# Optimization experiments

Measured on AMD Instinct MI355X. Metric: run time of the kernel, lower is better.

Reference implementation:

```python
import jax, jax.numpy as jnp
import numpy as np

D_MODEL = 256
N_HEADS = 4
WINDOW = 8
DECAY = 0.9
STEP_SIZE = 0.5


def _linear(x, w, b):
    # torch nn.Linear: y = x @ w.T + b, w: [out, in]
    return jnp.einsum('...i,oi->...o', x, w) + b


def _layernorm(x, scale, bias, eps=1e-5):
    mu = jnp.mean(x, axis=-1, keepdims=True)
    var = jnp.var(x, axis=-1, keepdims=True)
    return (x - mu) * jax.lax.rsqrt(var + eps) * scale + bias


def _ema(x, decay):
    # ema[t] = decay*ema[t-1] + (1-decay)*x[t], ema[-1]=0
    # (exactly the causal conv with weights (1-d)*d^i from the torch code)
    def step(c, xt):
        c = decay * c + (1.0 - decay) * xt
        return c, c
    _, ys = jax.lax.scan(step, jnp.zeros_like(x[:, 0]), jnp.swapaxes(x, 0, 1))
    return jnp.swapaxes(ys, 0, 1)


def setup_inputs() -> dict:
    key = jax.random.key(0)
    ks = iter(jax.random.split(key, 40))
    B, T, D = 8, 1024, D_MODEL
    s = 0.02
    inp = {
        'parallel_repr': jax.random.normal(next(ks), (B, T, D), jnp.float32),
        'sequential_state': jax.random.normal(next(ks), (B, D), jnp.float32),
        'trajectory_summary': jax.random.normal(next(ks), (B, D), jnp.float32),
        # MultiheadAttention params
        'in_proj_w': jax.random.normal(next(ks), (3 * D, D), jnp.float32) * s,
        'in_proj_b': jnp.zeros((3 * D,), jnp.float32),
        'out_proj_w': jax.random.normal(next(ks), (D, D), jnp.float32) * s,
        'out_proj_b': jnp.zeros((D,), jnp.float32),
        # depthwise causal conv (local history)
        'conv_w': jax.random.normal(next(ks), (D, 1, WINDOW), jnp.float32) * s,
        'conv_b': jnp.zeros((D,), jnp.float32),
        # parallel_to_sequential / sequential_to_parallel
        'p2s_w': jax.random.normal(next(ks), (D, D), jnp.float32) * s,
        'p2s_b': jnp.zeros((D,), jnp.float32),
        's2p_w': jax.random.normal(next(ks), (D, D), jnp.float32) * s,
        's2p_b': jnp.zeros((D,), jnp.float32),
        # transition MLP: 3D -> 2D -> D
        'trans_w1': jax.random.normal(next(ks), (2 * D, 3 * D), jnp.float32) * s,
        'trans_b1': jnp.zeros((2 * D,), jnp.float32),
        'trans_w2': jax.random.normal(next(ks), (D, 2 * D), jnp.float32) * s,
        'trans_b2': jnp.zeros((D,), jnp.float32),
        # FFN: D -> 4D -> D
        'ffn_w1': jax.random.normal(next(ks), (4 * D, D), jnp.float32) * s,
        'ffn_b1': jnp.zeros((4 * D,), jnp.float32),
        'ffn_w2': jax.random.normal(next(ks), (D, 4 * D), jnp.float32) * s,
        'ffn_b2': jnp.zeros((D,), jnp.float32),
        # LayerNorms
        'ln1_s': jnp.ones((D,), jnp.float32), 'ln1_b': jnp.zeros((D,), jnp.float32),
        'ln2_s': jnp.ones((D,), jnp.float32), 'ln2_b': jnp.zeros((D,), jnp.float32),
        'ln3_s': jnp.ones((D,), jnp.float32), 'ln3_b': jnp.zeros((D,), jnp.float32),
        'ln4_s': jnp.ones((D,), jnp.float32), 'ln4_b': jnp.zeros((D,), jnp.float32),
    }
    return inp


def _forward(parallel_repr, sequential_state,
             in_proj_w, in_proj_b, out_proj_w, out_proj_b,
             conv_w, conv_b, p2s_w, p2s_b, s2p_w, s2p_b,
             trans_w1, trans_b1, trans_w2, trans_b2,
             ffn_w1, ffn_b1, ffn_w2, ffn_b2,
             ln1_s, ln1_b, ln2_s, ln2_b, ln3_s, ln3_b, ln4_s, ln4_b):
    B, T, D = parallel_repr.shape
    H, hd = N_HEADS, D // N_HEADS

    # --- causal self-attention (nn.MultiheadAttention, batch_first) ---
    qkv = _linear(parallel_repr, in_proj_w, in_proj_b)
    q, k, v = jnp.split(qkv, 3, axis=-1)
    q = q.reshape(B, T, H, hd)
    k = k.reshape(B, T, H, hd)
    v = v.reshape(B, T, H, hd)
    scores = jnp.einsum('bqhd,bkhd->bhqk', q, k) / jnp.sqrt(jnp.asarray(hd, q.dtype))
    causal = jnp.triu(jnp.ones((T, T), bool), 1)
    scores = jnp.where(causal, jnp.finfo(scores.dtype).min, scores)
    attn = jax.nn.softmax(scores, axis=-1)
    attn_out = jnp.einsum('bhqk,bkhd->bqhd', attn, v).reshape(B, T, D)
    attn_out = _linear(attn_out, out_proj_w, out_proj_b)
    x = _layernorm(parallel_repr + attn_out, ln1_s, ln1_b)

    # --- depthwise causal conv (local history) ---
    xt = jnp.swapaxes(x, 1, 2)  # [B, D, T]
    xt_pad = jnp.pad(xt, ((0, 0), (0, 0), (WINDOW - 1, 0)))
    local = jax.lax.conv_general_dilated(
        xt_pad, conv_w, window_strides=(1,), padding='VALID',
        dimension_numbers=('NCH', 'OIH', 'NCH'), feature_group_count=D)
    local_history = jnp.swapaxes(local + conv_b[None, :, None], 1, 2)  # [B, T, D]

    # --- global EMA summary ---
    global_summary = _ema(x, DECAY)

    # --- transition deltas + cumsum state integration ---
    parallel_guidance = _linear(x, p2s_w, p2s_b)
    combined = jnp.concatenate([x + 0.3 * parallel_guidance, local_history, global_summary], axis=-1)
    h = jax.nn.gelu(_linear(combined, trans_w1, trans_b1), approximate=False)
    deltas = _linear(h, trans_w2, trans_b2)
    states = sequential_state[:, None, :] + jnp.cumsum(deltas, axis=1) * STEP_SIZE
    states = _layernorm(states, ln3_s, ln3_b)

    # --- FFN with sequential guidance ---
    seq_guidance = _linear(states, s2p_w, s2p_b)
    f = jax.nn.gelu(_linear(x + 0.3 * seq_guidance, ffn_w1, ffn_b1), approximate=False)
    ffn_out = _linear(f, ffn_w2, ffn_b2)
    x = _layernorm(x + ffn_out, ln2_s, ln2_b)

    final_sequential_state = _layernorm(states[:, -1, :], ln4_s, ln4_b)
    final_trajectory_summary = global_summary[:, -1, :]
    return x, final_sequential_state, final_trajectory_summary


def reference(parallel_repr, sequential_state, trajectory_summary,
              in_proj_w, in_proj_b, out_proj_w, out_proj_b,
              conv_w, conv_b, p2s_w, p2s_b, s2p_w, s2p_b,
              trans_w1, trans_b1, trans_w2, trans_b2,
              ffn_w1, ffn_b1, ffn_w2, ffn_b2,
              ln1_s, ln1_b, ln2_s, ln2_b, ln3_s, ln3_b, ln4_s, ln4_b):
    # trajectory_summary is accepted by the torch forward but never used.
    return _forward(parallel_repr, sequential_state,
                    in_proj_w, in_proj_b, out_proj_w, out_proj_b,
                    conv_w, conv_b, p2s_w, p2s_b, s2p_w, s2p_b,
                    trans_w1, trans_b1, trans_w2, trans_b2,
                    ffn_w1, ffn_b1, ffn_w2, ffn_b2,
                    ln1_s, ln1_b, ln2_s, ln2_b, ln3_s, ln3_b, ln4_s, ln4_b)
```

## Files before the change

### kernel.cpp

```cpp
#include <hip/hip_runtime.h>
#include <math.h>

typedef unsigned short u16;
typedef __attribute__((ext_vector_type(8))) short bf16x8;
typedef __attribute__((ext_vector_type(4))) float f32x4;

#define D_MODEL 256
#define T_SZ 1024
constexpr size_t S_ELT = (size_t)8192 * 256;
constexpr size_t MB = 1024 * 1024;

constexpr size_t OFF_QKV = 0;
constexpr size_t OFF_ATTN = 12 * MB;
constexpr size_t OFF_F = 0;
constexpr size_t OFF_X = 16 * MB;
constexpr size_t OFF_COMB = 24 * MB;
constexpr size_t OFF_FB = 36 * MB;
constexpr size_t OFF_H = 44 * MB;
constexpr size_t OFF_XBF = 48 * MB;
constexpr size_t OFF_WB = 52 * MB;
constexpr size_t OFF_SCR1 = 55 * MB;
constexpr size_t OFF_SCR2 = 55 * MB + 262144;

constexpr int WB_INPROJ = 0;
constexpr int WB_OUTPROJ = 196608;
constexpr int WB_P2S = 262144;
constexpr int WB_S2P = 327680;
constexpr int WB_T1 = 393216;
constexpr int WB_T2 = 786432;
constexpr int WB_F1 = 917504;
constexpr int WB_F2 = 1179648;
constexpr int WB_TOTAL = 1441792;
constexpr int PR_TOTAL = 2097152;

__device__ __forceinline__ u16 f2bf(float f) {
  unsigned int u = __float_as_uint(f);
  u += 0x7fff + ((u >> 16) & 1);
  return (u16)(u >> 16);
}
__device__ __forceinline__ float bf2f(u16 s) {
  return __uint_as_float(((unsigned int)s) << 16);
}

__device__ __forceinline__ void glds16(const u16* g, u16* l) {
  __builtin_amdgcn_global_load_lds(
      (const __attribute__((address_space(1))) void*)g,
      (__attribute__((address_space(3))) void*)l, 16, 0, 0);
}

__global__ __launch_bounds__(256)
void wconv_kernel(const float* w0, const float* w1, const float* w2,
                  const float* w3, const float* w4, const float* w5,
                  const float* w6, const float* w7, const float* pr,
                  u16* __restrict__ wb, u16* __restrict__ prb) {
  const int idx4 = (blockIdx.x * 256 + threadIdx.x) * 4;
  if (idx4 < WB_TOTAL) {
    const int offs[9] = {WB_INPROJ, WB_OUTPROJ, WB_P2S,  WB_S2P, WB_T1,
                         WB_T2,     WB_F1,      WB_F2,   WB_TOTAL};
    const float* srcs[8] = {w0, w1, w2, w3, w4, w5, w6, w7};
    int seg = 0;
    while (idx4 >= offs[seg + 1]) ++seg;
    float4 v = *(const float4*)(srcs[seg] + (idx4 - offs[seg]));
    unsigned int lo = (unsigned int)f2bf(v.x) | ((unsigned int)f2bf(v.y) << 16);
    unsigned int hi = (unsigned int)f2bf(v.z) | ((unsigned int)f2bf(v.w) << 16);
    *(uint2*)(wb + idx4) = make_uint2(lo, hi);
  } else {
    const int i4 = idx4 - WB_TOTAL;
    if (i4 < PR_TOTAL) {
      float4 v = *(const float4*)(pr + i4);
      unsigned int lo = (unsigned int)f2bf(v.x) | ((unsigned int)f2bf(v.y) << 16);
      unsigned int hi = (unsigned int)f2bf(v.z) | ((unsigned int)f2bf(v.w) << 16);
      *(uint2*)(prb + i4) = make_uint2(lo, hi);
    }
  }
}

enum { EPI_NONE = 0, EPI_GELU = 1, EPI_ADDSCALE = 2 };

template <int EPI, int BM, int BN, bool OUTBF, bool VSPLIT>
__global__ __launch_bounds__(256, 4)
void mgemm(const u16* __restrict__ A, int lda,
           const u16* __restrict__ Wb, int K, const float* __restrict__ bias,
           void* __restrict__ Cv, int ldc, int col_off,
           const float* __restrict__ addsrc, u16* __restrict__ vt) {
  __shared__ u16 As[BM * 64];
  __shared__ u16 Bs[BN * 64];
  const int tid = threadIdx.x;
  const int w = tid >> 6, lane = tid & 63;
  const int ln = lane & 15, quad = lane >> 4;
  const int m0 = blockIdx.x * BM;
  const int n0 = blockIdx.y * BN;
  constexpr int MT = (BM == 128) ? 2 : 1;
  const int wm = w * (MT * 16);
  constexpr int wn = 0;
  constexpr int APW = BM / 64;
  constexpr int BPW = BN / 64;

  f32x4 acc[MT][4] = {};

  const int grow = lane >> 2;
  const int gk8 = (lane & 3) * 8;

  for (int k0 = 0; k0 < K; k0 += 64) {
#pragma unroll
    for (int s = 0; s < 2; ++s) {
#pragma unroll
      for (int p = 0; p < APW; ++p) {
        const int g = w * APW + p;
        glds16(A + (size_t)(m0 + g * 16 + grow) * lda + k0 + s * 32 + gk8,
               As + s * BM * 32 + g * 512);
      }
#pragma unroll
      for (int p = 0; p < BPW; ++p) {
        const int g = w * BPW + p;
        glds16(Wb + (size_t)(n0 + g * 16 + grow) * K + k0 + s * 32 + gk8,
               Bs + s * BN * 32 + g * 512);
      }
    }
    __syncthreads();
#pragma unroll
    for (int s = 0; s < 2; ++s) {
      const u16* abase = As + s * BM * 32 + (wm >> 4) * 512 + ln * 32 + quad * 8;
      const u16* bbase = Bs + s * BN * 32 + ln * 32 + quad * 8;
      bf16x8 af[MT], bv[4];
#pragma unroll
      for (int i = 0; i < MT; ++i) af[i] = *(const bf16x8*)(abase + i * 512);
#pragma unroll
      for (int j = 0; j < 4; ++j) bv[j] = *(const bf16x8*)(bbase + j * 512);
#pragma unroll
      for (int i = 0; i < MT; ++i)
#pragma unroll
        for (int j = 0; j < 4; ++j)
          acc[i][j] = __builtin_amdgcn_mfma_f32_16x16x32_bf16(af[i], bv[j],
                                                              acc[i][j], 0, 0, 0);
    }
    __syncthreads();
  }

#pragma unroll
  for (int i = 0; i < MT; ++i)
#pragma unroll
    for (int j = 0; j < 4; ++j) {
      const int col = n0 + wn + j * 16 + ln;
      const float bsv = bias[col];
      const int row0 = m0 + wm + i * 16 + quad * 4;
      float vals[4];
#pragma unroll
      for (int r = 0; r < 4; ++r) {
        float v = acc[i][j][r] + bsv;
        if (EPI == EPI_GELU) v = 0.5f * v * (1.0f + erff(v * 0.70710678f));
        if (EPI == EPI_ADDSCALE)
          v = addsrc[(size_t)(row0 + r) * 256 + col] + 0.3f * v;
        vals[r] = v;
      }
      if (VSPLIT && col >= 512) {
        ushort4 pk;
        pk.x = f2bf(vals[0]); pk.y = f2bf(vals[1]);
        pk.z = f2bf(vals[2]); pk.w = f2bf(vals[3]);
        *(ushort4*)(vt + (size_t)((row0 >> 10) * 256 + (col - 512)) * T_SZ +
                    (row0 & 1023)) = pk;
      } else if (OUTBF) {
#pragma unroll
        for (int r = 0; r < 4; ++r)
          ((u16*)Cv)[(size_t)(row0 + r) * ldc + col_off + col] = f2bf(vals[r]);
      } else {
#pragma unroll
        for (int r = 0; r < 4; ++r)
          ((float*)Cv)[(size_t)(row0 + r) * ldc + col_off + col] = vals[r];
      }
    }
}

__global__ __launch_bounds__(256)
void attn_flash(const u16* __restrict__ qkv, const u16* __restrict__ vt,
                u16* __restrict__ outp) {
  __shared__ u16 Ps[4][16][72];
  const int tid = threadIdx.x;
  const int w = tid >> 6, lane = tid & 63;
  const int ln = lane & 15, quad = lane >> 4, kq8 = quad * 8;
  const int wu = blockIdx.x * 4 + w;
  const int bh = wu >> 6, s = wu & 63;
  const int qt = (s & 1) ? (63 - (s >> 1)) : (s >> 1);
  const int q0 = qt * 16;
  const int b = bh >> 2, h = bh & 3;
  const u16* base = qkv + (size_t)b * T_SZ * 768;
  const u16* vbase = vt + (size_t)bh * 64 * T_SZ;

  bf16x8 qf[2];
#pragma unroll
  for (int ks = 0; ks < 2; ++ks)
    qf[ks] = *(const bf16x8*)(base + (size_t)(q0 + ln) * 768 + h * 64 +
                              ks * 32 + kq8);
  const short ob = (short)0x3F80;
  const bf16x8 ones = {ob, ob, ob, ob, ob, ob, ob, ob};

  f32x4 O[4] = {};
  f32x4 l_acc = {};
  const int ntiles = (qt >> 2) + 1;
  for (int jt = 0; jt < ntiles; ++jt) {
    const int c0 = jt * 64;
    f32x4 sv[4] = {};
#pragma unroll
    for (int ks = 0; ks < 2; ++ks)
#pragma unroll
      for (int j = 0; j < 4; ++j) {
        bf16x8 kf = *(const bf16x8*)(base + (size_t)(c0 + j * 16 + ln) * 768 +
                                     256 + h * 64 + ks * 32 + kq8);
        sv[j] = __builtin_amdgcn_mfma_f32_16x16x32_bf16(qf[ks], kf, sv[j], 0, 0, 0);
      }
    const bool need_mask = (c0 + 63 > q0);
#pragma unroll
    for (int j = 0; j < 4; ++j)
#pragma unroll
      for (int r = 0; r < 4; ++r) {
        float p = __expf(sv[j][r] * 0.125f);
        if (need_mask && (c0 + j * 16 + ln > q0 + quad * 4 + r)) p = 0.f;
        Ps[w][quad * 4 + r][j * 16 + ln] = f2bf(p);
      }
#pragma unroll
    for (int ks = 0; ks < 2; ++ks) {
      bf16x8 pf = *(const bf16x8*)&Ps[w][ln][ks * 32 + kq8];
      l_acc = __builtin_amdgcn_mfma_f32_16x16x32_bf16(pf, ones, l_acc, 0, 0, 0);
#pragma unroll
      for (int j = 0; j < 4; ++j) {
        bf16x8 vf = *(const bf16x8*)(vbase + (size_t)(j * 16 + ln) * T_SZ +
                                     c0 + ks * 32 + kq8);
        O[j] = __builtin_amdgcn_mfma_f32_16x16x32_bf16(pf, vf, O[j], 0, 0, 0);
      }
    }
  }
  u16* op = outp + (size_t)b * T_SZ * 256;
#pragma unroll
  for (int r = 0; r < 4; ++r) {
    const float inv = 1.f / l_acc[r];
#pragma unroll
    for (int j = 0; j < 4; ++j)
      op[(size_t)(q0 + quad * 4 + r) * 256 + h * 64 + j * 16 + ln] =
          f2bf(O[j][r] * inv);
  }
}

__device__ __forceinline__ float block_reduce_sum(float v, float* tmp) {
#pragma unroll
  for (int o = 32; o > 0; o >>= 1) v += __shfl_down(v, o);
  const int lane = threadIdx.x & 63, wid = threadIdx.x >> 6;
  if (lane == 0) tmp[wid] = v;
  __syncthreads();
  v = tmp[0] + tmp[1] + tmp[2] + tmp[3];
  __syncthreads();
  return v;
}

__device__ __forceinline__ float ln_finish(float v, float s1, float s2,
                                           float g, float bb) {
  float mean = s1 * (1.f / 256.f);
  float var = s2 * (1.f / 256.f) - mean * mean;
  return (v - mean) * rsqrtf(var + 1e-5f) * g + bb;
}

__global__ __launch_bounds__(256)
void ln_add_kernel(const float* __restrict__ a, const float* __restrict__ addsrc,
                   const float* __restrict__ g, const float* __restrict__ bb,
                   float* __restrict__ outp, u16* __restrict__ obf) {
  __shared__ float tmp[4];
  const size_t row = blockIdx.x;
  const int d = threadIdx.x;
  float v = a[row * 256 + d] + addsrc[row * 256 + d];
  float s1 = block_reduce_sum(v, tmp);
  float s2 = block_reduce_sum(v * v, tmp);
  float y = ln_finish(v, s1, s2, g[d], bb[d]);
  outp[row * 256 + d] = y;
  if (obf) obf[row * 256 + d] = f2bf(y);
}

__global__ __launch_bounds__(256)
void ln3_states_kernel(const float* __restrict__ deltas, const float* __restrict__ scr,
                       const float* __restrict__ seq, const float* __restrict__ g,
                       const float* __restrict__ bb, u16* __restrict__ st) {
  __shared__ float tmp[4];
  const int row = blockIdx.x;
  const int b = row >> 10, t = row & 1023;
  const int d = threadIdx.x;
  float v = seq[b * 256 + d] +
            0.5f * (deltas[(size_t)row * 256 + d] +
                    scr[(size_t)(b * 32 + (t >> 5)) * 256 + d]);
  float s1 = block_reduce_sum(v, tmp);
  float s2 = block_reduce_sum(v * v, tmp);
  st[(size_t)row * 256 + d] = f2bf(ln_finish(v, s1, s2, g[d], bb[d]));
}

__global__ __launch_bounds__(256)
void ln4_kernel(const u16* __restrict__ st, const float* __restrict__ g,
                const float* __restrict__ bb, float* __restrict__ outp) {
  __shared__ float tmp[4];
  const int b = blockIdx.x, d = threadIdx.x;
  float v = bf2f(st[(size_t)(b * T_SZ + 1023) * 256 + d]);
  float s1 = block_reduce_sum(v, tmp);
  float s2 = block_reduce_sum(v * v, tmp);
  outp[b * 256 + d] = ln_finish(v, s1, s2, g[d], bb[d]);
}

__global__ __launch_bounds__(256)
void emaconv_kernel(const float* __restrict__ x, const float* __restrict__ cw,
                    const float* __restrict__ cb, u16* __restrict__ comb,
                    float* __restrict__ scr) {
  const int bc = blockIdx.x;
  const int b = bc >> 5, ch = bc & 31;
  const int d = threadIdx.x;
  const int t0 = ch * 32;
  float wreg[8];
#pragma unroll
  for (int j = 0; j < 8; ++j) wreg[j] = cw[d * 8 + j];
  const float bias = cb[d];
  float xw[8];
#pragma unroll
  for (int j = 0; j < 7; ++j) {
    const int ts = t0 - 7 + j;
    xw[j] = (ts >= 0) ? x[(size_t)(b * T_SZ + ts) * 256 + d] : 0.f;
  }
  float c = 0.f;
#pragma unroll
  for (int tl = 0; tl < 32; ++tl) {
    const size_t row = (size_t)(b * T_SZ + t0 + tl);
    xw[7] = x[row * 256 + d];
    float conv = bias;
#pragma unroll
    for (int j = 0; j < 8; ++j) conv = fmaf(xw[j], wreg[j], conv);
    c = 0.9f * c + 0.1f * xw[7];
    comb[row * 768 + 256 + d] = f2bf(conv);
    comb[row * 768 + 512 + d] = f2bf(c);
#pragma unroll
    for (int j = 0; j < 7; ++j) xw[j] = xw[j + 1];
  }
  scr[(size_t)bc * 256 + d] = c;
}

__global__ __launch_bounds__(256)
void ema_b_kernel(float* __restrict__ scr) {
  const int b = blockIdx.x, d = threadIdx.x;
  const float q32 = 0.03433683820292512f;
  float carry = 0.f;
  for (int ch = 0; ch < 32; ++ch) {
    const size_t idx = (size_t)(b * 32 + ch) * 256 + d;
    float e = scr[idx];
    scr[idx] = carry;
    carry = e + q32 * carry;
  }
}

__global__ __launch_bounds__(256)
void ema_c_kernel(u16* __restrict__ comb, const float* __restrict__ scr,
                  float* __restrict__ fts) {
  const int row = blockIdx.x;
  const int b = row >> 10, t = row & 1023;
  const int d = threadIdx.x;
  const int ch = t >> 5, tl = t & 31;
  float carry = scr[(size_t)(b * 32 + ch) * 256 + d];
  float l = bf2f(comb[(size_t)row * 768 + 512 + d]);
  float y = fmaf(__powf(0.9f, (float)(tl + 1)), carry, l);
  comb[(size_t)row * 768 + 512 + d] = f2bf(y);
  if (t == 1023) fts[b * 256 + d] = y;
}

__global__ __launch_bounds__(256)
void cs_a_kernel(float* __restrict__ deltas, float* __restrict__ scr) {
  const int bc = blockIdx.x;
  const int b = bc >> 5, ch = bc & 31;
  const int d = threadIdx.x;
  const int t0 = ch * 32;
  float c = 0.f;
  for (int tl = 0; tl < 32; ++tl) {
    const size_t idx = (size_t)(b * T_SZ + t0 + tl) * 256 + d;
    c += deltas[idx];
    deltas[idx] = c;
  }
  scr[(size_t)bc * 256 + d] = c;
}

__global__ __launch_bounds__(256)
void cs_b_kernel(float* __restrict__ scr) {
  const int b = blockIdx.x, d = threadIdx.x;
  float carry = 0.f;
  for (int ch = 0; ch < 32; ++ch) {
    const size_t idx = (size_t)(b * 32 + ch) * 256 + d;
    float e = scr[idx];
    scr[idx] = carry;
    carry += e;
  }
}

extern "C" void kernel_launch(void* const* d_in, const int* in_sizes, int n_in,
                              void* d_out, int out_size, void* d_ws,
                              size_t ws_size, hipStream_t stream) {
  (void)in_sizes; (void)n_in; (void)out_size; (void)ws_size;
  const float* parallel_repr = (const float*)d_in[0];
  const float* sequential_state = (const float*)d_in[1];
  const float* in_proj_b = (const float*)d_in[4];
  const float* out_proj_b = (const float*)d_in[6];
  const float* conv_w = (const float*)d_in[7];
  const float* conv_b = (const float*)d_in[8];
  const float* p2s_b = (const float*)d_in[10];
  const float* s2p_b = (const float*)d_in[12];
  const float* trans_b1 = (const float*)d_in[14];
  const float* trans_b2 = (const float*)d_in[16];
  const float* ffn_b1 = (const float*)d_in[18];
  const float* ffn_b2 = (const float*)d_in[20];
  const float* ln1_s = (const float*)d_in[21];
  const float* ln1_b = (const float*)d_in[22];
  const float* ln2_s = (const float*)d_in[23];
  const float* ln2_b = (const float*)d_in[24];
  const float* ln3_s = (const float*)d_in[25];
  const float* ln3_b = (const float*)d_in[26];
  const float* ln4_s = (const float*)d_in[27];
  const float* ln4_b = (const float*)d_in[28];

  char* ws = (char*)d_ws;
  u16* qkv_bf = (u16*)(ws + OFF_QKV);
  u16* attn_bf = (u16*)(ws + OFF_ATTN);
  u16* states_bf = (u16*)(ws + OFF_ATTN);
  u16* f_bf = (u16*)(ws + OFF_F);
  float* x = (float*)(ws + OFF_X);
  u16* comb = (u16*)(ws + OFF_COMB);
  u16* pr_bf = (u16*)(ws + OFF_COMB);
  u16* ffn_in = (u16*)(ws + OFF_COMB);
  float* fbuf = (float*)(ws + OFF_FB);
  u16* vt = (u16*)(ws + OFF_H);
  u16* h_bf = (u16*)(ws + OFF_H);
  u16* x_bf = (u16*)(ws + OFF_XBF);
  u16* wb = (u16*)(ws + OFF_WB);
  float* scr1 = (float*)(ws + OFF_SCR1);
  float* scr2 = (float*)(ws + OFF_SCR2);
  float* out = (float*)d_out;
  float* out_fss = out + S_ELT;
  float* out_fts = out + S_ELT + 2048;

  const dim3 blk(256);

  wconv_kernel<<<3456, blk, 0, stream>>>(
      (const float*)d_in[3], (const float*)d_in[5], (const float*)d_in[9],
      (const float*)d_in[11], (const float*)d_in[13], (const float*)d_in[15],
      (const float*)d_in[17], (const float*)d_in[19], parallel_repr, wb, pr_bf);
  mgemm<EPI_NONE, 128, 64, true, true><<<dim3(64, 12), blk, 0, stream>>>(
      pr_bf, 256, wb + WB_INPROJ, 256, in_proj_b, qkv_bf, 768, 0, nullptr, vt);
  attn_flash<<<512, blk, 0, stream>>>(qkv_bf, vt, attn_bf);
  mgemm<EPI_NONE, 64, 64, false, false><<<dim3(128, 4), blk, 0, stream>>>(
      attn_bf, 256, wb + WB_OUTPROJ, 256, out_proj_b, fbuf, 256, 0, nullptr,
      nullptr);
  ln_add_kernel<<<8192, blk, 0, stream>>>(parallel_repr, fbuf, ln1_s, ln1_b, x,
                                          x_bf);
  emaconv_kernel<<<256, blk, 0, stream>>>(x, conv_w, conv_b, comb, scr1);
  ema_b_kernel<<<8, blk, 0, stream>>>(scr1);
  ema_c_kernel<<<8192, blk, 0, stream>>>(comb, scr1, out_fts);
  mgemm<EPI_ADDSCALE, 64, 64, true, false><<<dim3(128, 4), blk, 0, stream>>>(
      x_bf, 256, wb + WB_P2S, 256, p2s_b, comb, 768, 0, x, nullptr);
  mgemm<EPI_GELU, 128, 64, true, false><<<dim3(64, 8), blk, 0, stream>>>(
      comb, 768, wb + WB_T1, 768, trans_b1, h_bf, 512, 0, nullptr, nullptr);
  mgemm<EPI_NONE, 64, 64, false, false><<<dim3(128, 4), blk, 0, stream>>>(
      h_bf, 512, wb + WB_T2, 512, trans_b2, fbuf, 256, 0, nullptr, nullptr);
  cs_a_kernel<<<256, blk, 0, stream>>>(fbuf, scr2);
  cs_b_kernel<<<8, blk, 0, stream>>>(scr2);
  ln3_states_kernel<<<8192, blk, 0, stream>>>(fbuf, scr2, sequential_state,
                                              ln3_s, ln3_b, states_bf);
  ln4_kernel<<<8, blk, 0, stream>>>(states_bf, ln4_s, ln4_b, out_fss);
  mgemm<EPI_ADDSCALE, 64, 64, true, false><<<dim3(128, 4), blk, 0, stream>>>(
      states_bf, 256, wb + WB_S2P, 256, s2p_b, ffn_in, 256, 0, x, nullptr);
  mgemm<EPI_GELU, 128, 64, true, false><<<dim3(64, 16), blk, 0, stream>>>(
      ffn_in, 256, wb + WB_F1, 256, ffn_b1, f_bf, 1024, 0, nullptr, nullptr);
  mgemm<EPI_NONE, 64, 64, false, false><<<dim3(128, 4), blk, 0, stream>>>(
      f_bf, 1024, wb + WB_F2, 1024, ffn_b2, fbuf, 256, 0, nullptr, nullptr);
  ln_add_kernel<<<8192, blk, 0, stream>>>(x, fbuf, ln2_s, ln2_b, out, nullptr);
}
```

Before: 276.3 us.

## Fold p2s/s2p linears into downstream weights and fuse layernorms into GEMM epilogues

Precomputes the combined weights trans_w1·p2s and ffn_w1·s2p (plus folded biases) on device, so the p2s and s2p GEMMs disappear. The following GEMMs instead read a two-part K split from x_bf plus comb or states. The out-proj and FFN2 GEMMs now use a full-width 256-column tile and apply residual add plus LayerNorm in the epilogue, which removes the separate ln_add kernels. ln4 is merged into the ln3 kernel, and the qkv buffer drops the V columns. The costs are an extra fold kernel of fp32 matvec-style work on every call, low occupancy for the 64x256 tiles, and bf16 rounding of the folded weights.

```diff
diff --git a/kernel.cpp b/kernel.cpp
--- a/kernel.cpp
+++ b/kernel.cpp
@@ -10,17 +10,23 @@
 constexpr size_t S_ELT = (size_t)8192 * 256;
 constexpr size_t MB = 1024 * 1024;
 
-constexpr size_t OFF_QKV = 0;
-constexpr size_t OFF_ATTN = 12 * MB;
+constexpr size_t OFF_QK = 0;
+constexpr size_t OFF_ATTN = 8 * MB;
 constexpr size_t OFF_F = 0;
+constexpr size_t OFF_VT = 16 * MB;
 constexpr size_t OFF_X = 16 * MB;
 constexpr size_t OFF_COMB = 24 * MB;
+constexpr size_t OFF_PRBF = 24 * MB;
+constexpr size_t OFF_XBF = 32 * MB;
 constexpr size_t OFF_FB = 36 * MB;
-constexpr size_t OFF_H = 44 * MB;
-constexpr size_t OFF_XBF = 48 * MB;
-constexpr size_t OFF_WB = 52 * MB;
-constexpr size_t OFF_SCR1 = 55 * MB;
-constexpr size_t OFF_SCR2 = 55 * MB + 262144;
+constexpr size_t OFF_WB = 44 * MB;
+constexpr size_t OFF_W1X = OFF_WB + 2883584;
+constexpr size_t OFF_W1S = OFF_W1X + 262144;
+constexpr size_t OFF_SCR = OFF_W1S + 524288;
+constexpr size_t OFF_B1X = OFF_SCR + 262144;
+constexpr size_t OFF_B1S = OFF_B1X + 2048;
+constexpr size_t OFF_H = 48 * MB;
+constexpr size_t OFF_STATES = 48 * MB;
 
 constexpr int WB_INPROJ = 0;
 constexpr int WB_OUTPROJ = 196608;
@@ -46,6 +52,17 @@
   __builtin_amdgcn_global_load_lds(
       (const __attribute__((address_space(1))) void*)g,
       (__attribute__((address_space(3))) void*)l, 16, 0, 0);
+}
+
+__device__ __forceinline__ float block_reduce_sum(float v, float* tmp) {
+#pragma unroll
+  for (int o = 32; o > 0; o >>= 1) v += __shfl_down(v, o);
+  const int lane = threadIdx.x & 63, wid = threadIdx.x >> 6;
+  if (lane == 0) tmp[wid] = v;
+  __syncthreads();
+  v = tmp[0] + tmp[1] + tmp[2] + tmp[3];
+  __syncthreads();
+  return v;
 }
 
 __global__ __launch_bounds__(256)
@@ -75,14 +92,46 @@
   }
 }
 
-enum { EPI_NONE = 0, EPI_GELU = 1, EPI_ADDSCALE = 2 };
+__global__ __launch_bounds__(256)
+void wfold_kernel(const float* __restrict__ t1, const float* __restrict__ tb1,
+                  const float* __restrict__ p2s, const float* __restrict__ p2sb,
+                  const float* __restrict__ f1, const float* __restrict__ fb1,
+                  const float* __restrict__ s2p, const float* __restrict__ s2pb,
+                  u16* __restrict__ w1x, u16* __restrict__ w1s,
+                  float* __restrict__ b1x, float* __restrict__ b1s) {
+  __shared__ float tmp[4];
+  const int n = blockIdx.x, i = threadIdx.x;
+  if (n < 512) {
+    const float* arow = t1 + (size_t)n * 768;
+    float acc = 0.f;
+#pragma unroll 8
+    for (int k = 0; k < 256; ++k) acc = fmaf(arow[k], p2s[k * 256 + i], acc);
+    w1x[n * 256 + i] = f2bf(arow[i] + 0.3f * acc);
+    float s = block_reduce_sum(arow[i] * p2sb[i], tmp);
+    if (i == 0) b1x[n] = tb1[n] + 0.3f * s;
+  } else {
+    const int m = n - 512;
+    const float* arow = f1 + (size_t)m * 256;
+    float acc = 0.f;
+#pragma unroll 8
+    for (int k = 0; k < 256; ++k) acc = fmaf(arow[k], s2p[k * 256 + i], acc);
+    w1s[m * 256 + i] = f2bf(0.3f * acc);
+    float s = block_reduce_sum(arow[i] * s2pb[i], tmp);
+    if (i == 0) b1s[m] = fb1[m] + 0.3f * s;
+  }
+}
+
+enum { EPI_NONE = 0, EPI_GELU = 1, EPI_LN = 2 };
 
 template <int EPI, int BM, int BN, bool OUTBF, bool VSPLIT>
-__global__ __launch_bounds__(256, 4)
-void mgemm(const u16* __restrict__ A, int lda,
-           const u16* __restrict__ Wb, int K, const float* __restrict__ bias,
-           void* __restrict__ Cv, int ldc, int col_off,
-           const float* __restrict__ addsrc, u16* __restrict__ vt) {
+__global__ __launch_bounds__(256, (BN == 256 ? 1 : 4))
+void mgemm(const u16* __restrict__ A1, int lda1, const u16* __restrict__ A2,
+           int lda2, int ksplit, const u16* __restrict__ W1, int ldw1,
+           const u16* __restrict__ W2, int ldw2, int woff2, int K,
+           const float* __restrict__ bias, void* __restrict__ Cv, int ldc,
+           const float* __restrict__ addsrc, const float* __restrict__ lng,
+           const float* __restrict__ lnb, u16* __restrict__ obf,
+           u16* __restrict__ vt) {
   __shared__ u16 As[BM * 64];
   __shared__ u16 Bs[BN * 64];
   const int tid = threadIdx.x;
@@ -90,13 +139,13 @@
   const int ln = lane & 15, quad = lane >> 4;
   const int m0 = blockIdx.x * BM;
   const int n0 = blockIdx.y * BN;
-  constexpr int MT = (BM == 128) ? 2 : 1;
+  constexpr int MT = BM / 64;
+  constexpr int NT = BN / 16;
   const int wm = w * (MT * 16);
-  constexpr int wn = 0;
   constexpr int APW = BM / 64;
   constexpr int BPW = BN / 64;
 
-  f32x4 acc[MT][4] = {};
+  f32x4 acc[MT][NT] = {};
 
   const int grow = lane >> 2;
   const int gk8 = (lane & 3) * 8;
@@ -104,16 +153,24 @@
   for (int k0 = 0; k0 < K; k0 += 64) {
 #pragma unroll
     for (int s = 0; s < 2; ++s) {
+      const int kb = k0 + s * 32;
+      const bool r1 = kb < ksplit;
+      const u16* Ab = r1 ? A1 : A2;
+      const int alda = r1 ? lda1 : lda2;
+      const int ak = r1 ? kb : kb - ksplit;
 #pragma unroll
       for (int p = 0; p < APW; ++p) {
         const int g = w * APW + p;
-        glds16(A + (size_t)(m0 + g * 16 + grow) * lda + k0 + s * 32 + gk8,
+        glds16(Ab + (size_t)(m0 + g * 16 + grow) * alda + ak + gk8,
                As + s * BM * 32 + g * 512);
       }
+      const u16* Wb = r1 ? W1 : W2;
+      const int wlda = r1 ? ldw1 : ldw2;
+      const int wk = r1 ? kb : kb - woff2;
 #pragma unroll
       for (int p = 0; p < BPW; ++p) {
         const int g = w * BPW + p;
-        glds16(Wb + (size_t)(n0 + g * 16 + grow) * K + k0 + s * 32 + gk8,
+        glds16(Wb + (size_t)(n0 + g * 16 + grow) * wlda + wk + gk8,
                Bs + s * BN * 32 + g * 512);
       }
     }
@@ -122,26 +179,66 @@
     for (int s = 0; s < 2; ++s) {
       const u16* abase = As + s * BM * 32 + (wm >> 4) * 512 + ln * 32 + quad * 8;
       const u16* bbase = Bs + s * BN * 32 + ln * 32 + quad * 8;
-      bf16x8 af[MT], bv[4];
+      bf16x8 af[MT], bv[NT];
 #pragma unroll
       for (int i = 0; i < MT; ++i) af[i] = *(const bf16x8*)(abase + i * 512);
 #pragma unroll
-      for (int j = 0; j < 4; ++j) bv[j] = *(const bf16x8*)(bbase + j * 512);
+      for (int j = 0; j < NT; ++j) bv[j] = *(const bf16x8*)(bbase + j * 512);
 #pragma unroll
       for (int i = 0; i < MT; ++i)
 #pragma unroll
-        for (int j = 0; j < 4; ++j)
+        for (int j = 0; j < NT; ++j)
           acc[i][j] = __builtin_amdgcn_mfma_f32_16x16x32_bf16(af[i], bv[j],
                                                               acc[i][j], 0, 0, 0);
     }
     __syncthreads();
   }
 
+  if (EPI == EPI_LN) {
+    float vals[NT][4];
+    float s1[4] = {}, s2[4] = {};
+#pragma unroll
+    for (int j = 0; j < NT; ++j) {
+      const int col = j * 16 + ln;
+      const float bsv = bias[col];
+      const int row0 = m0 + wm + quad * 4;
+#pragma unroll
+      for (int r = 0; r < 4; ++r) {
+        float v = acc[0][j][r] + bsv + addsrc[(size_t)(row0 + r) * 256 + col];
+        vals[j][r] = v;
+        s1[r] += v;
+        s2[r] += v * v;
+      }
+    }
+#pragma unroll
+    for (int r = 0; r < 4; ++r)
+#pragma unroll
+      for (int m = 1; m <= 8; m <<= 1) {
+        s1[r] += __shfl_xor(s1[r], m, 64);
+        s2[r] += __shfl_xor(s2[r], m, 64);
+      }
+#pragma unroll
+    for (int r = 0; r < 4; ++r) {
+      const int row = m0 + wm + quad * 4 + r;
+      const float mean = s1[r] * (1.f / 256.f);
+      const float var = s2[r] * (1.f / 256.f) - mean * mean;
+      const float rstd = rsqrtf(var + 1e-5f);
+#pragma unroll
+      for (int j = 0; j < NT; ++j) {
+        const int col = j * 16 + ln;
+        float y = (vals[j][r] - mean) * rstd * lng[col] + lnb[col];
+        ((float*)Cv)[(size_t)row * 256 + col] = y;
+        if (obf) obf[(size_t)row * 256 + col] = f2bf(y);
+      }
+    }
+    return;
+  }
+
 #pragma unroll
   for (int i = 0; i < MT; ++i)
 #pragma unroll
-    for (int j = 0; j < 4; ++j) {
-      const int col = n0 + wn + j * 16 + ln;
+    for (int j = 0; j < NT; ++j) {
+      const int col = n0 + j * 16 + ln;
       const float bsv = bias[col];
       const int row0 = m0 + wm + i * 16 + quad * 4;
       float vals[4];
@@ -149,8 +246,6 @@
       for (int r = 0; r < 4; ++r) {
         float v = acc[i][j][r] + bsv;
         if (EPI == EPI_GELU) v = 0.5f * v * (1.0f + erff(v * 0.70710678f));
-        if (EPI == EPI_ADDSCALE)
-          v = addsrc[(size_t)(row0 + r) * 256 + col] + 0.3f * v;
         vals[r] = v;
       }
       if (VSPLIT && col >= 512) {
@@ -162,17 +257,17 @@
       } else if (OUTBF) {
 #pragma unroll
         for (int r = 0; r < 4; ++r)
-          ((u16*)Cv)[(size_t)(row0 + r) * ldc + col_off + col] = f2bf(vals[r]);
+          ((u16*)Cv)[(size_t)(row0 + r) * ldc + col] = f2bf(vals[r]);
       } else {
 #pragma unroll
         for (int r = 0; r < 4; ++r)
-          ((float*)Cv)[(size_t)(row0 + r) * ldc + col_off + col] = vals[r];
-      }
-    }
-}
-
-__global__ __launch_bounds__(256)
-void attn_flash(const u16* __restrict__ qkv, const u16* __restrict__ vt,
+          ((float*)Cv)[(size_t)(row0 + r) * ldc + col] = vals[r];
+      }
+    }
+}
+
+__global__ __launch_bounds__(256)
+void attn_flash(const u16* __restrict__ qk, const u16* __restrict__ vt,
                 u16* __restrict__ outp) {
   __shared__ u16 Ps[4][16][72];
   const int tid = threadIdx.x;
@@ -183,13 +278,13 @@
   const int qt = (s & 1) ? (63 - (s >> 1)) : (s >> 1);
   const int q0 = qt * 16;
   const int b = bh >> 2, h = bh & 3;
-  const u16* base = qkv + (size_t)b * T_SZ * 768;
+  const u16* base = qk + (size_t)b * T_SZ * 512;
   const u16* vbase = vt + (size_t)bh * 64 * T_SZ;
 
   bf16x8 qf[2];
 #pragma unroll
   for (int ks = 0; ks < 2; ++ks)
-    qf[ks] = *(const bf16x8*)(base + (size_t)(q0 + ln) * 768 + h * 64 +
+    qf[ks] = *(const bf16x8*)(base + (size_t)(q0 + ln) * 512 + h * 64 +
                               ks * 32 + kq8);
   const short ob = (short)0x3F80;
   const bf16x8 ones = {ob, ob, ob, ob, ob, ob, ob, ob};
@@ -204,7 +299,7 @@
     for (int ks = 0; ks < 2; ++ks)
 #pragma unroll
       for (int j = 0; j < 4; ++j) {
-        bf16x8 kf = *(const bf16x8*)(base + (size_t)(c0 + j * 16 + ln) * 768 +
+        bf16x8 kf = *(const bf16x8*)(base + (size_t)(c0 + j * 16 + ln) * 512 +
                                      256 + h * 64 + ks * 32 + kq8);
         sv[j] = __builtin_amdgcn_mfma_f32_16x16x32_bf16(qf[ks], kf, sv[j], 0, 0, 0);
       }
@@ -238,17 +333,6 @@
       op[(size_t)(q0 + quad * 4 + r) * 256 + h * 64 + j * 16 + ln] =
           f2bf(O[j][r] * inv);
   }
-}
-
-__device__ __forceinline__ float block_reduce_sum(float v, float* tmp) {
-#pragma unroll
-  for (int o = 32; o > 0; o >>= 1) v += __shfl_down(v, o);
-  const int lane = threadIdx.x & 63, wid = threadIdx.x >> 6;
-  if (lane == 0) tmp[wid] = v;
-  __syncthreads();
-  v = tmp[0] + tmp[1] + tmp[2] + tmp[3];
-  __syncthreads();
-  return v;
 }
 
 __device__ __forceinline__ float ln_finish(float v, float s1, float s2,
@@ -259,24 +343,11 @@
 }
 
 __global__ __launch_bounds__(256)
-void ln_add_kernel(const float* __restrict__ a, const float* __restrict__ addsrc,
-                   const float* __restrict__ g, const float* __restrict__ bb,
-                   float* __restrict__ outp, u16* __restrict__ obf) {
-  __shared__ float tmp[4];
-  const size_t row = blockIdx.x;
-  const int d = threadIdx.x;
-  float v = a[row * 256 + d] + addsrc[row * 256 + d];
-  float s1 = block_reduce_sum(v, tmp);
-  float s2 = block_reduce_sum(v * v, tmp);
-  float y = ln_finish(v, s1, s2, g[d], bb[d]);
-  outp[row * 256 + d] = y;
-  if (obf) obf[row * 256 + d] = f2bf(y);
-}
-
-__global__ __launch_bounds__(256)
-void ln3_states_kernel(const float* __restrict__ deltas, const float* __restrict__ scr,
-                       const float* __restrict__ seq, const float* __restrict__ g,
-                       const float* __restrict__ bb, u16* __restrict__ st) {
+void ln34_kernel(const float* __restrict__ deltas, const float* __restrict__ scr,
+                 const float* __restrict__ seq, const float* __restrict__ g3,
+                 const float* __restrict__ b3, const float* __restrict__ g4,
+                 const float* __restrict__ b4, u16* __restrict__ st,
+                 float* __restrict__ fss) {
   __shared__ float tmp[4];
   const int row = blockIdx.x;
   const int b = row >> 10, t = row & 1023;
@@ -286,18 +357,13 @@
                     scr[(size_t)(b * 32 + (t >> 5)) * 256 + d]);
   float s1 = block_reduce_sum(v, tmp);
   float s2 = block_reduce_sum(v * v, tmp);
-  st[(size_t)row * 256 + d] = f2bf(ln_finish(v, s1, s2, g[d], bb[d]));
-}
-
-__global__ __launch_bounds__(256)
-void ln4_kernel(const u16* __restrict__ st, const float* __restrict__ g,
-                const float* __restrict__ bb, float* __restrict__ outp) {
-  __shared__ float tmp[4];
-  const int b = blockIdx.x, d = threadIdx.x;
-  float v = bf2f(st[(size_t)(b * T_SZ + 1023) * 256 + d]);
-  float s1 = block_reduce_sum(v, tmp);
-  float s2 = block_reduce_sum(v * v, tmp);
-  outp[b * 256 + d] = ln_finish(v, s1, s2, g[d], bb[d]);
+  float y = ln_finish(v, s1, s2, g3[d], b3[d]);
+  st[(size_t)row * 256 + d] = f2bf(y);
+  if (t == 1023) {
+    float t1s = block_reduce_sum(y, tmp);
+    float t2s = block_reduce_sum(y * y, tmp);
+    fss[b * 256 + d] = ln_finish(y, t1s, t2s, g4[d], b4[d]);
+  }
 }
 
 __global__ __launch_bounds__(256)
@@ -327,8 +393,8 @@
 #pragma unroll
     for (int j = 0; j < 8; ++j) conv = fmaf(xw[j], wreg[j], conv);
     c = 0.9f * c + 0.1f * xw[7];
-    comb[row * 768 + 256 + d] = f2bf(conv);
-    comb[row * 768 + 512 + d] = f2bf(c);
+    comb[row * 512 + d] = f2bf(conv);
+    comb[row * 512 + 256 + d] = f2bf(c);
 #pragma unroll
     for (int j = 0; j < 7; ++j) xw[j] = xw[j + 1];
   }
@@ -356,9 +422,9 @@
   const int d = threadIdx.x;
   const int ch = t >> 5, tl = t & 31;
   float carry = scr[(size_t)(b * 32 + ch) * 256 + d];
-  float l = bf2f(comb[(size_t)row * 768 + 512 + d]);
+  float l = bf2f(comb[(size_t)row * 512 + 256 + d]);
   float y = fmaf(__powf(0.9f, (float)(tl + 1)), carry, l);
-  comb[(size_t)row * 768 + 512 + d] = f2bf(y);
+  comb[(size_t)row * 512 + 256 + d] = f2bf(y);
   if (t == 1023) fts[b * 256 + d] = y;
 }
 
@@ -415,21 +481,23 @@
   const float* ln4_b = (const float*)d_in[28];
 
   char* ws = (char*)d_ws;
-  u16* qkv_bf = (u16*)(ws + OFF_QKV);
+  u16* qk_bf = (u16*)(ws + OFF_QK);
   u16* attn_bf = (u16*)(ws + OFF_ATTN);
-  u16* states_bf = (u16*)(ws + OFF_ATTN);
   u16* f_bf = (u16*)(ws + OFF_F);
+  u16* vt = (u16*)(ws + OFF_VT);
   float* x = (float*)(ws + OFF_X);
   u16* comb = (u16*)(ws + OFF_COMB);
-  u16* pr_bf = (u16*)(ws + OFF_COMB);
-  u16* ffn_in = (u16*)(ws + OFF_COMB);
+  u16* pr_bf = (u16*)(ws + OFF_PRBF);
+  u16* x_bf = (u16*)(ws + OFF_XBF);
   float* fbuf = (float*)(ws + OFF_FB);
-  u16* vt = (u16*)(ws + OFF_H);
+  u16* wb = (u16*)(ws + OFF_WB);
+  u16* w1x = (u16*)(ws + OFF_W1X);
+  u16* w1s = (u16*)(ws + OFF_W1S);
+  float* scr = (float*)(ws + OFF_SCR);
+  float* b1x = (float*)(ws + OFF_B1X);
+  float* b1s = (float*)(ws + OFF_B1S);
   u16* h_bf = (u16*)(ws + OFF_H);
-  u16* x_bf = (u16*)(ws + OFF_XBF);
-  u16* wb = (u16*)(ws + OFF_WB);
-  float* scr1 = (float*)(ws + OFF_SCR1);
-  float* scr2 = (float*)(ws + OFF_SCR2);
+  u16* states_bf = (u16*)(ws + OFF_STATES);
   float* out = (float*)d_out;
   float* out_fss = out + S_ELT;
   float* out_fts = out + S_ELT + 2048;
@@ -440,33 +508,34 @@
       (const float*)d_in[3], (const float*)d_in[5], (const float*)d_in[9],
       (const float*)d_in[11], (const float*)d_in[13], (const float*)d_in[15],
       (const float*)d_in[17], (const float*)d_in[19], parallel_repr, wb, pr_bf);
+  wfold_kernel<<<1536, blk, 0, stream>>>(
+      (const float*)d_in[13], trans_b1, (const float*)d_in[9], p2s_b,
+      (const float*)d_in[17], ffn_b1, (const float*)d_in[11], s2p_b,
+      w1x, w1s, b1x, b1s);
   mgemm<EPI_NONE, 128, 64, true, true><<<dim3(64, 12), blk, 0, stream>>>(
-      pr_bf, 256, wb + WB_INPROJ, 256, in_proj_b, qkv_bf, 768, 0, nullptr, vt);
-  attn_flash<<<512, blk, 0, stream>>>(qkv_bf, vt, attn_bf);
+      pr_bf, 256, nullptr, 0, 256, wb + WB_INPROJ, 256, nullptr, 0, 0, 256,
+      in_proj_b, qk_bf, 512, nullptr, nullptr, nullptr, nullptr, vt);
+  attn_flash<<<512, blk, 0, stream>>>(qk_bf, vt, attn_bf);
+  mgemm<EPI_LN, 64, 256, false, false><<<dim3(128, 1), blk, 0, stream>>>(
+      attn_bf, 256, nullptr, 0, 256, wb + WB_OUTPROJ, 256, nullptr, 0, 0, 256,
+      out_proj_b, x, 256, parallel_repr, ln1_s, ln1_b, x_bf, nullptr);
+  emaconv_kernel<<<256, blk, 0, stream>>>(x, conv_w, conv_b, comb, scr);
+  ema_b_kernel<<<8, blk, 0, stream>>>(scr);
+  ema_c_kernel<<<8192, blk, 0, stream>>>(comb, scr, out_fts);
+  mgemm<EPI_GELU, 128, 64, true, false><<<dim3(64, 8), blk, 0, stream>>>(
+      x_bf, 256, comb, 512, 256, w1x, 256, wb + WB_T1, 768, 0, 768, b1x, h_bf,
+      512, nullptr, nullptr, nullptr, nullptr, nullptr);
   mgemm<EPI_NONE, 64, 64, false, false><<<dim3(128, 4), blk, 0, stream>>>(
-      attn_bf, 256, wb + WB_OUTPROJ, 256, out_proj_b, fbuf, 256, 0, nullptr,
-      nullptr);
-  ln_add_kernel<<<8192, blk, 0, stream>>>(parallel_repr, fbuf, ln1_s, ln1_b, x,
-                                          x_bf);
-  emaconv_kernel<<<256, blk, 0, stream>>>(x, conv_w, conv_b, comb, scr1);
-  ema_b_kernel<<<8, blk, 0, stream>>>(scr1);
-  ema_c_kernel<<<8192, blk, 0, stream>>>(comb, scr1, out_fts);
-  mgemm<EPI_ADDSCALE, 64, 64, true, false><<<dim3(128, 4), blk, 0, stream>>>(
-      x_bf, 256, wb + WB_P2S, 256, p2s_b, comb, 768, 0, x, nullptr);
-  mgemm<EPI_GELU, 128, 64, true, false><<<dim3(64, 8), blk, 0, stream>>>(
-      comb, 768, wb + WB_T1, 768, trans_b1, h_bf, 512, 0, nullptr, nullptr);
-  mgemm<EPI_NONE, 64, 64, false, false><<<dim3(128, 4), blk, 0, stream>>>(
-      h_bf, 512, wb + WB_T2, 512, trans_b2, fbuf, 256, 0, nullptr, nullptr);
-  cs_a_kernel<<<256, blk, 0, stream>>>(fbuf, scr2);
-  cs_b_kernel<<<8, blk, 0, stream>>>(scr2);
-  ln3_states_kernel<<<8192, blk, 0, stream>>>(fbuf, scr2, sequential_state,
-                                              ln3_s, ln3_b, states_bf);
-  ln4_kernel<<<8, blk, 0, stream>>>(states_bf, ln4_s, ln4_b, out_fss);
-  mgemm<EPI_ADDSCALE, 64, 64, true, false><<<dim3(128, 4), blk, 0, stream>>>(
-      states_bf, 256, wb + WB_S2P, 256, s2p_b, ffn_in, 256, 0, x, nullptr);
+      h_bf, 512, nullptr, 0, 512, wb + WB_T2, 512, nullptr, 0, 0, 512,
+      trans_b2, fbuf, 256, nullptr, nullptr, nullptr, nullptr, nullptr);
+  cs_a_kernel<<<256, blk, 0, stream>>>(fbuf, scr);
+  cs_b_kernel<<<8, blk, 0, stream>>>(scr);
+  ln34_kernel<<<8192, blk, 0, stream>>>(fbuf, scr, sequential_state, ln3_s,
+                                        ln3_b, ln4_s, ln4_b, states_bf, out_fss);
   mgemm<EPI_GELU, 128, 64, true, false><<<dim3(64, 16), blk, 0, stream>>>(
-      ffn_in, 256, wb + WB_F1, 256, ffn_b1, f_bf, 1024, 0, nullptr, nullptr);
-  mgemm<EPI_NONE, 64, 64, false, false><<<dim3(128, 4), blk, 0, stream>>>(
-      f_bf, 1024, wb + WB_F2, 1024, ffn_b2, fbuf, 256, 0, nullptr, nullptr);
-  ln_add_kernel<<<8192, blk, 0, stream>>>(x, fbuf, ln2_s, ln2_b, out, nullptr);
-}
+      x_bf, 256, states_bf, 256, 256, wb + WB_F1, 256, w1s, 256, 256, 512, b1s,
+      f_bf, 1024, nullptr, nullptr, nullptr, nullptr, nullptr);
+  mgemm<EPI_LN, 64, 256, false, false><<<dim3(128, 1), blk, 0, stream>>>(
+      f_bf, 1024, nullptr, 0, 1024, wb + WB_F2, 1024, nullptr, 0, 0, 1024,
+      ffn_b2, out, 256, x, ln2_s, ln2_b, nullptr, nullptr);
+}
```

Result: slower. 302.0 us (+9.3%).
